# Kernel optimization log

Measured on AMD Instinct MI355X. Metric: run time of the kernel, lower is better.

Reference implementation:

```python
import jax, jax.numpy as jnp
import numpy as np

C = 256   # hidden_size (in_channels)
V = 97    # VOC_SIZE + 1
T = 32    # encoder time steps
N = 4096  # batch of text instances


def setup_inputs() -> dict:
    key = jax.random.key(0)
    ks = jax.random.split(key, 10)
    s = lambda k, shape: jax.random.normal(k, shape, dtype=jnp.float32) * 0.05
    return {
        "input": jax.random.randint(ks[0], (N,), 0, V),
        "hidden": s(ks[1], (1, N, C)),
        "encoder_outputs": s(ks[2], (T, N, C)),
        "emb": s(ks[3], (V, C)),
        "combine_w": s(ks[4], (C, 2 * C)), "combine_b": jnp.zeros((C,), jnp.float32),
        "vat_w": s(ks[5], (1, C)), "vat_b": jnp.zeros((1,), jnp.float32),
        "gru_w_ih": s(ks[6], (3 * C, C)), "gru_w_hh": s(ks[7], (3 * C, C)),
        "gru_b_ih": jnp.zeros((3 * C,), jnp.float32), "gru_b_hh": jnp.zeros((3 * C,), jnp.float32),
        "out_w": s(ks[8], (V, C)), "out_b": jnp.zeros((V,), jnp.float32),
    }


def reference(input, hidden, encoder_outputs, emb, combine_w, combine_b,
              vat_w, vat_b, gru_w_ih, gru_w_hh, gru_b_ih, gru_b_hh,
              out_w, out_b):
    # Embedding lookup (dropout = identity in eval mode)
    embedded = emb[input]                                   # [N, C]

    # Bahdanau additive attention: vat(tanh(hidden + enc))
    alpha = jnp.tanh(hidden + encoder_outputs)              # [T, N, C]
    scores = jnp.einsum('tnc,c->nt', alpha, vat_w[0]) + vat_b[0]  # [N, T]
    attn = jax.nn.softmax(scores, axis=1)                   # [N, T]
    applied = jnp.einsum('nt,tnc->nc', attn, encoder_outputs)     # [N, C]

    # Combine + relu
    x = jnp.concatenate([embedded, applied], axis=1) @ combine_w.T + combine_b  # [N, C]
    x = jax.nn.relu(x)

    # Single-step GRU cell (PyTorch gate ordering: r, z, n)
    h = hidden[0]                                           # [N, C]
    gi = x @ gru_w_ih.T + gru_b_ih                          # [N, 3C]
    gh = h @ gru_w_hh.T + gru_b_hh                          # [N, 3C]
    ir, iz, i_n = jnp.split(gi, 3, axis=1)
    hr, hz, h_n = jnp.split(gh, 3, axis=1)
    r = jax.nn.sigmoid(ir + hr)
    z = jax.nn.sigmoid(iz + hz)
    n = jnp.tanh(i_n + r * h_n)
    h_new = (1.0 - z) * n + z * h                           # [N, C]

    out = jax.nn.log_softmax(h_new @ out_w.T + out_b, axis=1)  # [N, V]
    return out, h_new[None, :, :], attn[:, None, :]
```

## Files before the change

kernel.cpp:

```cpp
#include <hip/hip_runtime.h>

typedef unsigned short u16;
typedef unsigned int u32;
using bf16x8 = __attribute__((ext_vector_type(8))) __bf16;
using f32x4  = __attribute__((ext_vector_type(4))) float;

__device__ __forceinline__ u16 f2bf(float f) {
  union { float f; unsigned int i; } v; v.f = f;
  unsigned int r = v.i + 0x7fffu + ((v.i >> 16) & 1u);
  return (u16)(r >> 16);
}
__device__ __forceinline__ void cvt8(u16* dst, const float* src) {
  float4 a0 = *reinterpret_cast<const float4*>(src);
  float4 a1 = *reinterpret_cast<const float4*>(src + 4);
  dst[0] = f2bf(a0.x); dst[1] = f2bf(a0.y); dst[2] = f2bf(a0.z); dst[3] = f2bf(a0.w);
  dst[4] = f2bf(a1.x); dst[5] = f2bf(a1.y); dst[6] = f2bf(a1.z); dst[7] = f2bf(a1.w);
}
__device__ __forceinline__ float ftanh(float x) {
  float e = __expf(2.f * x);
  return 1.f - 2.f / (e + 1.f);
}
__device__ __forceinline__ float fsigm(float x) {
  return 1.f / (1.f + __expf(-x));
}
__device__ __forceinline__ float ptanh(float x) {
  const float c1 = -0.3333333333f, c2 = 0.1333333333f, c3 = -0.0539682540f;
  float t = x * x;
  float r = __builtin_fmaf(__builtin_fmaf(c3, t, c2), t, c1);
  return __builtin_fmaf(x * t, r, x);
}

__global__ __launch_bounds__(256) void k_prep(
    const float* __restrict__ cw, const float* __restrict__ wih,
    const float* __restrict__ whh, const float* __restrict__ ow,
    u16* __restrict__ Wc, u16* __restrict__ Wi,
    u16* __restrict__ Wh, u16* __restrict__ Wo)
{
  int id = blockIdx.x * 256 + threadIdx.x;
  u16 tmp[8];
  if (id < 16384) {
    cvt8(tmp, &cw[id * 8]);
    *reinterpret_cast<uint4*>(&Wc[id * 8]) = *reinterpret_cast<const uint4*>(tmp);
  } else if (id < 40960) {
    int c = id - 16384;
    cvt8(tmp, &wih[c * 8]);
    *reinterpret_cast<uint4*>(&Wi[c * 8]) = *reinterpret_cast<const uint4*>(tmp);
  } else if (id < 65536) {
    int c = id - 40960;
    cvt8(tmp, &whh[c * 8]);
    *reinterpret_cast<uint4*>(&Wh[c * 8]) = *reinterpret_cast<const uint4*>(tmp);
  } else {
    int c = id - 65536;
    int row = c >> 5, col = (c & 31) * 8;
    if (row < 97) {
      cvt8(tmp, &ow[row * 256 + col]);
    } else {
      #pragma unroll
      for (int i = 0; i < 8; ++i) tmp[i] = 0;
    }
    *reinterpret_cast<uint4*>(&Wo[c * 8]) = *reinterpret_cast<const uint4*>(tmp);
  }
}

__global__ __launch_bounds__(256) void k_attn(
    const float* __restrict__ enc, const float* __restrict__ hid,
    const float* __restrict__ vw,  const float* __restrict__ emb,
    const int* __restrict__ inp,
    float* __restrict__ out_attn, u16* __restrict__ Acomb)
{
  __shared__ float a_s[4][256];
  __shared__ float es_s[32];
  __shared__ float l_s[4];

  const int n   = blockIdx.x;
  const int tid = threadIdx.x;
  const int w   = tid >> 6;
  const int ln  = tid & 63;
  const int c0  = ln * 4;

  const float4 h  = *reinterpret_cast<const float4*>(&hid[(size_t)n * 256 + c0]);
  const float4 wv = *reinterpret_cast<const float4*>(&vw[c0]);

  float a0 = 0.f, a1 = 0.f, a2 = 0.f, a3 = 0.f, l = 0.f;
  const float* ep = &enc[(size_t)n * 256 + c0];

  #pragma unroll
  for (int j = 0; j < 8; ++j) {
    const int t = w * 8 + j;
    const float4 e = *reinterpret_cast<const float4*>(ep + (size_t)t * 1048576);
    float s;
    s = ptanh(h.x + e.x) * wv.x;
    s = __builtin_fmaf(ptanh(h.y + e.y), wv.y, s);
    s = __builtin_fmaf(ptanh(h.z + e.z), wv.z, s);
    s = __builtin_fmaf(ptanh(h.w + e.w), wv.w, s);
    #pragma unroll
    for (int k = 32; k >= 1; k >>= 1) s += __shfl_xor(s, k, 64);
    float ex = __expf(s);
    l += ex;
    a0 = __builtin_fmaf(ex, e.x, a0); a1 = __builtin_fmaf(ex, e.y, a1);
    a2 = __builtin_fmaf(ex, e.z, a2); a3 = __builtin_fmaf(ex, e.w, a3);
    if (ln == 0) es_s[t] = ex;
  }

  *reinterpret_cast<float4*>(&a_s[w][c0]) = make_float4(a0, a1, a2, a3);
  if (ln == 0) l_s[w] = l;
  __syncthreads();

  {
    const int c = tid;
    float lt = (l_s[0] + l_s[1]) + (l_s[2] + l_s[3]);
    float at = (a_s[0][c] + a_s[1][c]) + (a_s[2][c] + a_s[3][c]);
    Acomb[(size_t)n * 512 + 256 + c] = f2bf(at / lt);
    float em = emb[(size_t)inp[n] * 256 + c];
    Acomb[(size_t)n * 512 + c] = f2bf(em);
    if (c < 32) out_attn[(size_t)n * 32 + c] = es_s[c] / lt;
  }
}

__global__ __launch_bounds__(512) void k_rest(
    const float* __restrict__ hid, const u16* __restrict__ Acomb,
    const u16* __restrict__ Wc, const u16* __restrict__ Wi,
    const u16* __restrict__ Wh, const u16* __restrict__ Wo,
    const float* __restrict__ cb, const float* __restrict__ bih,
    const float* __restrict__ bhh, const float* __restrict__ bo,
    float* __restrict__ out_logits, float* __restrict__ out_h)
{
  __shared__ __attribute__((aligned(16))) u16 Ac_s[16 * 16 * 40];
  __shared__ __attribute__((aligned(16))) u16 Hb_s[8 * 16 * 40];
  __shared__ __attribute__((aligned(16))) u16 X_s [8 * 16 * 40];
  __shared__ __attribute__((aligned(16))) u16 Hn_s[8 * 16 * 40];
  __shared__ float L_s[16 * 113];

  const int tid = threadIdx.x;
  const int n0  = blockIdx.x * 16;

  #pragma unroll
  for (int i = 0; i < 2; ++i) {
    int idx = tid + i * 512;
    int row = idx >> 6, q = idx & 63;
    *reinterpret_cast<uint4*>(&Ac_s[((q >> 2) * 16 + row) * 40 + (q & 3) * 8]) =
      *reinterpret_cast<const uint4*>(&Acomb[(size_t)(n0 + row) * 512 + q * 8]);
  }
  {
    int row = tid >> 5, q = tid & 31;
    cvt8(&Hb_s[((q >> 2) * 16 + row) * 40 + (q & 3) * 8],
         &hid[(size_t)(n0 + row) * 256 + q * 8]);
  }
  __syncthreads();

  const int wave = tid >> 6, lane = tid & 63;
  const int lr = lane & 15, quad = lane >> 4;

  {
    f32x4 accB[2] = {};
    const u16* wp = &Wc[(size_t)(wave * 32 + lr) * 512 + quad * 8];
    #pragma unroll
    for (int kt = 0; kt < 16; ++kt) {
      bf16x8 aF = *reinterpret_cast<const bf16x8*>(&Ac_s[(kt * 16 + lr) * 40 + quad * 8]);
      bf16x8 b0 = *reinterpret_cast<const bf16x8*>(&wp[kt * 32]);
      bf16x8 b1 = *reinterpret_cast<const bf16x8*>(&wp[16 * 512 + kt * 32]);
      accB[0] = __builtin_amdgcn_mfma_f32_16x16x32_bf16(aF, b0, accB[0], 0, 0, 0);
      accB[1] = __builtin_amdgcn_mfma_f32_16x16x32_bf16(aF, b1, accB[1], 0, 0, 0);
    }
    #pragma unroll
    for (int sn = 0; sn < 2; ++sn) {
      int col = wave * 32 + sn * 16 + lr;
      float bv = cb[col];
      #pragma unroll
      for (int r = 0; r < 4; ++r) {
        float v = fmaxf(accB[sn][r] + bv, 0.f);
        X_s[((col >> 5) * 16 + quad * 4 + r) * 40 + (col & 31)] = f2bf(v);
      }
    }
  }
  __syncthreads();

  {
    f32x4 aI[3][2] = {};
    f32x4 aH[3][2] = {};
    const int c0w = wave * 32;
    const u16* baseI = &Wi[(size_t)(c0w + lr) * 256 + quad * 8];
    const u16* baseH = &Wh[(size_t)(c0w + lr) * 256 + quad * 8];
    #pragma unroll
    for (int kt = 0; kt < 8; ++kt) {
      bf16x8 xF = *reinterpret_cast<const bf16x8*>(&X_s [(kt * 16 + lr) * 40 + quad * 8]);
      bf16x8 hF = *reinterpret_cast<const bf16x8*>(&Hb_s[(kt * 16 + lr) * 40 + quad * 8]);
      #pragma unroll
      for (int g = 0; g < 3; ++g) {
        #pragma unroll
        for (int sn = 0; sn < 2; ++sn) {
          const size_t off = (size_t)(g * 256 + sn * 16) * 256 + kt * 32;
          bf16x8 bI = *reinterpret_cast<const bf16x8*>(&baseI[off]);
          bf16x8 bH = *reinterpret_cast<const bf16x8*>(&baseH[off]);
          aI[g][sn] = __builtin_amdgcn_mfma_f32_16x16x32_bf16(xF, bI, aI[g][sn], 0, 0, 0);
          aH[g][sn] = __builtin_amdgcn_mfma_f32_16x16x32_bf16(hF, bH, aH[g][sn], 0, 0, 0);
        }
      }
    }
    #pragma unroll
    for (int sn = 0; sn < 2; ++sn) {
      int gc = c0w + sn * 16 + lr;
      float b_ir = bih[gc],       b_hr = bhh[gc];
      float b_iz = bih[256 + gc], b_hz = bhh[256 + gc];
      float b_in = bih[512 + gc], b_hn = bhh[512 + gc];
      #pragma unroll
      for (int r = 0; r < 4; ++r) {
        int row = quad * 4 + r;
        float rg = fsigm(aI[0][sn][r] + b_ir + aH[0][sn][r] + b_hr);
        float zg = fsigm(aI[1][sn][r] + b_iz + aH[1][sn][r] + b_hz);
        float ng = ftanh(aI[2][sn][r] + b_in + rg * (aH[2][sn][r] + b_hn));
        float hv = hid[(size_t)(n0 + row) * 256 + gc];
        float hn = (1.f - zg) * ng + zg * hv;
        out_h[(size_t)(n0 + row) * 256 + gc] = hn;
        Hn_s[((gc >> 5) * 16 + row) * 40 + (gc & 31)] = f2bf(hn);
      }
    }
  }
  __syncthreads();

  if (wave < 7) {
    f32x4 accO = {};
    const u16* wp = &Wo[(size_t)(wave * 16 + lr) * 256 + quad * 8];
    #pragma unroll
    for (int kt = 0; kt < 8; ++kt) {
      bf16x8 aF = *reinterpret_cast<const bf16x8*>(&Hn_s[(kt * 16 + lr) * 40 + quad * 8]);
      bf16x8 bF = *reinterpret_cast<const bf16x8*>(&wp[kt * 32]);
      accO = __builtin_amdgcn_mfma_f32_16x16x32_bf16(aF, bF, accO, 0, 0, 0);
    }
    int col = wave * 16 + lr;
    if (col < 97) {
      float bv = bo[col];
      #pragma unroll
      for (int r = 0; r < 4; ++r)
        L_s[(quad * 4 + r) * 113 + col] = accO[r] + bv;
    }
  }
  __syncthreads();

  {
    int row = tid >> 5, p = tid & 31;
    float m = -1e30f, l = 0.f;
    for (int c = p; c < 97; c += 32) {
      float v = L_s[row * 113 + c];
      if (v > m) { l = l * __expf(m - v) + 1.f; m = v; }
      else l += __expf(v - m);
    }
    #pragma unroll
    for (int k = 16; k >= 1; k >>= 1) {
      float m2 = __shfl_xor(m, k, 64);
      float l2 = __shfl_xor(l, k, 64);
      if (m2 > m) { l = l * __expf(m - m2) + l2; m = m2; }
      else l += l2 * __expf(m2 - m);
    }
    float lz = m + __logf(l);
    for (int c = p; c < 97; c += 32)
      out_logits[(size_t)(n0 + row) * 97 + c] = L_s[row * 113 + c] - lz;
  }
}

extern "C" void kernel_launch(void* const* d_in, const int* in_sizes, int n_in,
                              void* d_out, int out_size, void* d_ws, size_t ws_size,
                              hipStream_t stream) {
  const int*   inp = (const int*)d_in[0];
  const float* hid = (const float*)d_in[1];
  const float* enc = (const float*)d_in[2];
  const float* emb = (const float*)d_in[3];
  const float* cw  = (const float*)d_in[4];
  const float* cb  = (const float*)d_in[5];
  const float* vw  = (const float*)d_in[6];
  const float* wih = (const float*)d_in[8];
  const float* whh = (const float*)d_in[9];
  const float* bih = (const float*)d_in[10];
  const float* bhh = (const float*)d_in[11];
  const float* ow  = (const float*)d_in[12];
  const float* ob  = (const float*)d_in[13];

  float* out        = (float*)d_out;
  float* out_logits = out;
  float* out_h      = out + 4096 * 97;
  float* out_attn   = out_h + 4096 * 256;

  u16* Acomb = (u16*)d_ws;
  u16* Wc = Acomb + 4096 * 512;
  u16* Wi = Wc + 131072;
  u16* Wh = Wi + 196608;
  u16* Wo = Wh + 196608;

  k_prep<<<270, 256, 0, stream>>>(cw, wih, whh, ow, Wc, Wi, Wh, Wo);
  k_attn<<<4096, 256, 0, stream>>>(enc, hid, vw, emb, inp, out_attn, Acomb);
  k_rest<<<256, 512, 0, stream>>>(hid, Acomb, Wc, Wi, Wh, Wo,
                                  cb, bih, bhh, ob, out_logits, out_h);
}
```

Before: 259.5 us.

## Fuse weight conversion into attention kernel and batch encoder loads

Folds the weight-to-bf16 conversion kernel into the first 270 blocks of the attention kernel, removing one launch and its serialization gap. The attention loop is restructured so all eight encoder float4 loads are issued up front, then the scores are computed and their eight shuffle-reduction chains run interleaved, giving more memory-level parallelism and ILP. It also adds a launch-bounds occupancy hint of 4 blocks. In exchange each thread holds more registers for the buffered loads, and the early blocks do extra conversion work before their attention work.

```diff
diff --git a/kernel.cpp b/kernel.cpp
--- a/kernel.cpp
+++ b/kernel.cpp
@@ -30,43 +30,15 @@
   return __builtin_fmaf(x * t, r, x);
 }
 
-__global__ __launch_bounds__(256) void k_prep(
-    const float* __restrict__ cw, const float* __restrict__ wih,
-    const float* __restrict__ whh, const float* __restrict__ ow,
-    u16* __restrict__ Wc, u16* __restrict__ Wi,
-    u16* __restrict__ Wh, u16* __restrict__ Wo)
-{
-  int id = blockIdx.x * 256 + threadIdx.x;
-  u16 tmp[8];
-  if (id < 16384) {
-    cvt8(tmp, &cw[id * 8]);
-    *reinterpret_cast<uint4*>(&Wc[id * 8]) = *reinterpret_cast<const uint4*>(tmp);
-  } else if (id < 40960) {
-    int c = id - 16384;
-    cvt8(tmp, &wih[c * 8]);
-    *reinterpret_cast<uint4*>(&Wi[c * 8]) = *reinterpret_cast<const uint4*>(tmp);
-  } else if (id < 65536) {
-    int c = id - 40960;
-    cvt8(tmp, &whh[c * 8]);
-    *reinterpret_cast<uint4*>(&Wh[c * 8]) = *reinterpret_cast<const uint4*>(tmp);
-  } else {
-    int c = id - 65536;
-    int row = c >> 5, col = (c & 31) * 8;
-    if (row < 97) {
-      cvt8(tmp, &ow[row * 256 + col]);
-    } else {
-      #pragma unroll
-      for (int i = 0; i < 8; ++i) tmp[i] = 0;
-    }
-    *reinterpret_cast<uint4*>(&Wo[c * 8]) = *reinterpret_cast<const uint4*>(tmp);
-  }
-}
-
-__global__ __launch_bounds__(256) void k_attn(
+__global__ __launch_bounds__(256, 4) void k_attn(
     const float* __restrict__ enc, const float* __restrict__ hid,
     const float* __restrict__ vw,  const float* __restrict__ emb,
     const int* __restrict__ inp,
-    float* __restrict__ out_attn, u16* __restrict__ Acomb)
+    const float* __restrict__ cw,  const float* __restrict__ wih,
+    const float* __restrict__ whh, const float* __restrict__ ow,
+    float* __restrict__ out_attn,  u16* __restrict__ Acomb,
+    u16* __restrict__ Wc, u16* __restrict__ Wi,
+    u16* __restrict__ Wh, u16* __restrict__ Wo)
 {
   __shared__ float a_s[4][256];
   __shared__ float es_s[32];
@@ -74,32 +46,79 @@
 
   const int n   = blockIdx.x;
   const int tid = threadIdx.x;
-  const int w   = tid >> 6;
-  const int ln  = tid & 63;
-  const int c0  = ln * 4;
+
+  if (blockIdx.x < 270) {
+    int id = blockIdx.x * 256 + tid;
+    u16 tmp[8];
+    if (id < 16384) {
+      cvt8(tmp, &cw[id * 8]);
+      *reinterpret_cast<uint4*>(&Wc[id * 8]) = *reinterpret_cast<const uint4*>(tmp);
+    } else if (id < 40960) {
+      int c = id - 16384;
+      cvt8(tmp, &wih[c * 8]);
+      *reinterpret_cast<uint4*>(&Wi[c * 8]) = *reinterpret_cast<const uint4*>(tmp);
+    } else if (id < 65536) {
+      int c = id - 40960;
+      cvt8(tmp, &whh[c * 8]);
+      *reinterpret_cast<uint4*>(&Wh[c * 8]) = *reinterpret_cast<const uint4*>(tmp);
+    } else {
+      int c = id - 65536;
+      int row = c >> 5, col = (c & 31) * 8;
+      if (row < 97) {
+        cvt8(tmp, &ow[row * 256 + col]);
+      } else {
+        #pragma unroll
+        for (int i = 0; i < 8; ++i) tmp[i] = 0;
+      }
+      *reinterpret_cast<uint4*>(&Wo[c * 8]) = *reinterpret_cast<const uint4*>(tmp);
+    }
+  }
+
+  const int w  = tid >> 6;
+  const int ln = tid & 63;
+  const int c0 = ln * 4;
 
   const float4 h  = *reinterpret_cast<const float4*>(&hid[(size_t)n * 256 + c0]);
   const float4 wv = *reinterpret_cast<const float4*>(&vw[c0]);
-
-  float a0 = 0.f, a1 = 0.f, a2 = 0.f, a3 = 0.f, l = 0.f;
   const float* ep = &enc[(size_t)n * 256 + c0];
 
+  float4 E[8];
+  #pragma unroll
+  for (int j = 0; j < 8; ++j)
+    E[j] = *reinterpret_cast<const float4*>(ep + (size_t)(w * 8 + j) * 1048576);
+
+  float s[8];
   #pragma unroll
   for (int j = 0; j < 8; ++j) {
-    const int t = w * 8 + j;
-    const float4 e = *reinterpret_cast<const float4*>(ep + (size_t)t * 1048576);
-    float s;
-    s = ptanh(h.x + e.x) * wv.x;
-    s = __builtin_fmaf(ptanh(h.y + e.y), wv.y, s);
-    s = __builtin_fmaf(ptanh(h.z + e.z), wv.z, s);
-    s = __builtin_fmaf(ptanh(h.w + e.w), wv.w, s);
-    #pragma unroll
-    for (int k = 32; k >= 1; k >>= 1) s += __shfl_xor(s, k, 64);
-    float ex = __expf(s);
-    l += ex;
-    a0 = __builtin_fmaf(ex, e.x, a0); a1 = __builtin_fmaf(ex, e.y, a1);
-    a2 = __builtin_fmaf(ex, e.z, a2); a3 = __builtin_fmaf(ex, e.w, a3);
-    if (ln == 0) es_s[t] = ex;
+    float v;
+    v = ptanh(h.x + E[j].x) * wv.x;
+    v = __builtin_fmaf(ptanh(h.y + E[j].y), wv.y, v);
+    v = __builtin_fmaf(ptanh(h.z + E[j].z), wv.z, v);
+    v = __builtin_fmaf(ptanh(h.w + E[j].w), wv.w, v);
+    s[j] = v;
+  }
+
+  #pragma unroll
+  for (int k = 32; k >= 1; k >>= 1) {
+    #pragma unroll
+    for (int j = 0; j < 8; ++j) s[j] += __shfl_xor(s[j], k, 64);
+  }
+
+  float l = 0.f;
+  #pragma unroll
+  for (int j = 0; j < 8; ++j) { s[j] = __expf(s[j]); l += s[j]; }
+  if (ln == 0) {
+    #pragma unroll
+    for (int j = 0; j < 8; ++j) es_s[w * 8 + j] = s[j];
+  }
+
+  float a0 = 0.f, a1 = 0.f, a2 = 0.f, a3 = 0.f;
+  #pragma unroll
+  for (int j = 0; j < 8; ++j) {
+    a0 = __builtin_fmaf(s[j], E[j].x, a0);
+    a1 = __builtin_fmaf(s[j], E[j].y, a1);
+    a2 = __builtin_fmaf(s[j], E[j].z, a2);
+    a3 = __builtin_fmaf(s[j], E[j].w, a3);
   }
 
   *reinterpret_cast<float4*>(&a_s[w][c0]) = make_float4(a0, a1, a2, a3);
@@ -286,8 +305,9 @@
   u16* Wh = Wi + 196608;
   u16* Wo = Wh + 196608;
 
-  k_prep<<<270, 256, 0, stream>>>(cw, wih, whh, ow, Wc, Wi, Wh, Wo);
-  k_attn<<<4096, 256, 0, stream>>>(enc, hid, vw, emb, inp, out_attn, Acomb);
+  k_attn<<<4096, 256, 0, stream>>>(enc, hid, vw, emb, inp,
+                                   cw, wih, whh, ow,
+                                   out_attn, Acomb, Wc, Wi, Wh, Wo);
   k_rest<<<256, 512, 0, stream>>>(hid, Acomb, Wc, Wi, Wh, Wo,
                                   cb, bih, bhh, ob, out_logits, out_h);
 }
```

Result: no change. 260.2 us (+0.2%).
